# Kernel tuning notes

Measured on AMD Instinct MI355X. Metric: run time of the kernel, lower is better.

The kernel has to match this reference:

```python
import jax, jax.numpy as jnp
import numpy as np

N = 5000       # num_vertices
E = 160000     # num edges (avg degree 32)
F = 256        # per-node feature width
T = 8          # T_train iterative steps
LR_X = 0.1
N_INTERNAL = 2500


def setup_inputs() -> dict:
    key = jax.random.key(0)
    k1, k2, k3 = jax.random.split(key, 3)
    values = jax.random.normal(k1, (N, F), dtype=jnp.float32)
    w = jax.random.normal(k2, (N, N), dtype=jnp.float32) * 0.05  # nn.init.normal_(std=0.05)
    edge_index = jax.random.randint(k3, (2, E), 0, N, dtype=jnp.int64)
    internal_indices = jnp.arange(N_INTERNAL, dtype=jnp.int64)
    return {"values": values, "w": w, "edge_index": edge_index,
            "internal_indices": internal_indices}


def reference(values, w, edge_index, internal_indices):
    # PyG source_to_target flow: x_j = x[edge_index[0]], aggregate at edge_index[1]
    src, dst = edge_index[0], edge_index[1]
    w_e = w[src, dst][:, None]            # [E,1] gathered edge weights
    lr = jnp.float32(LR_X)

    def step(vals, _):
        # prediction_mp: scatter_add of w * tanh(x_j) into dst
        pred = jax.ops.segment_sum(w_e * jnp.tanh(vals[src]), dst, num_segments=N)
        err = vals - pred                 # errors[:] = values - prediction
        # gradx_mp: scatter_add of w * dfdx(err_j); dfdx(tanh) = 1 - tanh^2
        t = jnp.tanh(err[src])
        gradx = err - jax.ops.segment_sum(w_e * (1.0 - t * t), dst, num_segments=N)
        # values[internal] -= lr_x * dEdx[internal]  (train=True mask)
        vals = vals.at[internal_indices].add(-lr * gradx[internal_indices])
        return vals, None

    vals, _ = jax.lax.scan(step, values, None, length=T)
    return vals
```

## Files before the change

kernel.cpp:

```cpp
#include <hip/hip_runtime.h>
#include <hip/hip_bf16.h>

#define FDIM 256
#define F2   128
#define T_STEPS 8
#define LR_X 0.1f
#define EXT_BIT (1 << 24)

typedef __hip_bfloat162 bf2;

__device__ __forceinline__ float ftanh(float x) {
    float ax = fabsf(x);
    float z  = __expf(-2.f * ax);
    float t  = (1.f - z) * __builtin_amdgcn_rcpf(1.f + z);
    return copysignf(t, x);
}
__device__ __forceinline__ float2 bf22f(const bf2 v) {
    return make_float2(__bfloat162float(v.x), __bfloat162float(v.y));
}
__device__ __forceinline__ bf2 f22bf(float x, float y) {
    bf2 r; r.x = __float2bfloat16(x); r.y = __float2bfloat16(y); return r;
}


__global__ void k_count_init(const int* __restrict__ dst, int* __restrict__ cnt, int E,
                             const float* __restrict__ vin, float* __restrict__ vals,
                             bf2* __restrict__ th2, int NF2, int gE) {
    const int b = (int)blockIdx.x;
    if (b < gE) {
        int e = b * 256 + (int)threadIdx.x;
        if (e < E) atomicAdd(&cnt[dst[e]], 1);
    } else {
        int i = (b - gE) * 256 + (int)threadIdx.x;
        if (i < NF2) {
            float2 v = ((const float2*)vin)[i];
            ((float2*)vals)[i] = v;
            th2[i] = f22bf(ftanh(v.x), ftanh(v.y));
        }
    }
}

__global__ __launch_bounds__(1024) void k_scan(int* cntcur, int* start, int n) {
    __shared__ int sdata[1024];
    int running = 0;
    for (int base = 0; base < n + 1; base += 1024) {
        int i = base + (int)threadIdx.x;
        int v = (i < n) ? cntcur[i] : 0;
        sdata[threadIdx.x] = v;
        __syncthreads();
        for (int off = 1; off < 1024; off <<= 1) {
            int t = ((int)threadIdx.x >= off) ? sdata[threadIdx.x - off] : 0;
            __syncthreads();
            sdata[threadIdx.x] += t;
            __syncthreads();
        }
        int incl = sdata[threadIdx.x];
        int total = sdata[1023];
        if (i <= n) {
            int excl = running + incl - v;
            start[i] = excl;
            if (i < n) cntcur[i] = excl;
        }
        running += total;
        __syncthreads();
    }
}

__global__ void k_fill(const int* __restrict__ src, const int* __restrict__ dst,
                       int* __restrict__ cursor, int* __restrict__ keyT,
                       int* __restrict__ colS, int E, int NI) {
    int e = blockIdx.x * blockDim.x + threadIdx.x;
    if (e >= E) return;
    int sc = src[e];
    int p = atomicAdd(&cursor[dst[e]], 1);
    keyT[p] = ((sc >= NI) ? EXT_BIT : 0) | e;
    colS[p] = sc;
}

__global__ __launch_bounds__(256) void k_rank_scatter(
    const int* __restrict__ keyT, const int* __restrict__ colS,
    const int* __restrict__ start, const float* __restrict__ w,
    int* __restrict__ col, float* __restrict__ wv, int* __restrict__ mid,
    int nRows, int N) {
    const int wid  = (int)((blockIdx.x * blockDim.x + threadIdx.x) >> 6);
    const int lane = (int)(threadIdx.x & 63);
    if (wid >= nRows) return;
    const int s = start[wid], e = start[wid + 1];
    int nInt = 0;
    for (int i = s + lane; i < e; i += 64) {
        const int myk = keyT[i];
        int rank = 0;
        for (int j = s; j < e; ++j)
            rank += (keyT[j] < myk) ? 1 : 0;
        const int pos = s + rank;
        const int sc  = colS[i];
        col[pos] = sc * F2;
        wv[pos]  = w[(size_t)sc * N + wid];
        nInt += (myk < EXT_BIT) ? 1 : 0;
    }
    for (int off = 1; off < 64; off <<= 1)
        nInt += __shfl_xor(nInt, off);
    if (lane == 0) mid[wid] = s + nInt;
}


__device__ __forceinline__ void gather_acc(
    const int* __restrict__ col, const float* __restrict__ wv,
    const bf2* __restrict__ src2, int s, int e, int lane, int f,
    float& ax, float& ay, float& bx, float& by) {
    for (int base = s; base < e; base += 64) {
        const int n = min(64, e - base);
        int c = 0; float ww = 0.f;
        if (lane < n) { c = col[base + lane]; ww = wv[base + lane]; }
        int j = 0;
        for (; j + 2 <= n; j += 2) {
            const int   c0 = __shfl(c, j),  c1 = __shfl(c, j + 1);
            const float w0 = __shfl(ww, j), w1 = __shfl(ww, j + 1);
            const float2 t0 = bf22f(src2[c0 + f]);
            const float2 t1 = bf22f(src2[c1 + f]);
            ax = fmaf(w0, t0.x, ax); ay = fmaf(w0, t0.y, ay);
            bx = fmaf(w1, t1.x, bx); by = fmaf(w1, t1.y, by);
        }
        for (; j < n; ++j) {
            const int c0 = __shfl(c, j); const float w0 = __shfl(ww, j);
            const float2 t0 = bf22f(src2[c0 + f]);
            ax = fmaf(w0, t0.x, ax); ay = fmaf(w0, t0.y, ay);
        }
    }
}

__global__ __launch_bounds__(F2) void k_pred_first(
    const int* __restrict__ start, const int* __restrict__ mid,
    const int* __restrict__ col, const float* __restrict__ wv,
    const float2* __restrict__ vals2, float2* __restrict__ predc2,
    const bf2* __restrict__ th2, float2* __restrict__ err2,
    bf2* __restrict__ dd2, int NI) {
    const int d = (int)blockIdx.x;
    const int f = (int)threadIdx.x;
    const int lane = f & 63;
    const int s = start[d], m = mid[d], e = start[d + 1];
    float ix = 0.f, iy = 0.f, jx = 0.f, jy = 0.f;
    float xx = 0.f, xy = 0.f, yx = 0.f, yy = 0.f;
    gather_acc(col, wv, th2, s, m, lane, f, ix, iy, jx, jy);
    gather_acc(col, wv, th2, m, e, lane, f, xx, xy, yx, yy);
    const int idx = d * F2 + f;
    const float pcx = xx + yx, pcy = xy + yy;
    predc2[idx] = make_float2(pcx, pcy);
    const float2 v = vals2[idx];
    const float ex = v.x - (pcx + ix + jx);
    const float ey = v.y - (pcy + iy + jy);
    if (d < NI) err2[idx] = make_float2(ex, ey);
    const float ux = ftanh(ex), uy = ftanh(ey);
    dd2[idx] = f22bf(1.f - ux * ux, 1.f - uy * uy);
}

__global__ __launch_bounds__(F2) void k_pred(
    const int* __restrict__ start, const int* __restrict__ mid,
    const int* __restrict__ col, const float* __restrict__ wv,
    const float2* __restrict__ vals2, const float2* __restrict__ predc2,
    const bf2* __restrict__ th2, float2* __restrict__ err2,
    bf2* __restrict__ dd2, int NI) {
    const int d = (int)blockIdx.x;
    const int f = (int)threadIdx.x;
    const int lane = f & 63;
    const int s = start[d], m = mid[d];
    float ax = 0.f, ay = 0.f, bx = 0.f, by = 0.f;
    gather_acc(col, wv, th2, s, m, lane, f, ax, ay, bx, by);
    const int idx = d * F2 + f;
    const float2 pc = predc2[idx];
    const float2 v  = vals2[idx];
    const float ex = v.x - (pc.x + ax + bx);
    const float ey = v.y - (pc.y + ay + by);
    if (d < NI) err2[idx] = make_float2(ex, ey);
    const float ux = ftanh(ex), uy = ftanh(ey);
    dd2[idx] = f22bf(1.f - ux * ux, 1.f - uy * uy);
}

__global__ __launch_bounds__(F2) void k_grad(
    const int* __restrict__ start, const int* __restrict__ col,
    const float* __restrict__ wv, const float2* __restrict__ err2,
    const bf2* __restrict__ dd2, float2* __restrict__ vals2,
    bf2* __restrict__ th2) {
    const int d = (int)blockIdx.x;
    const int f = (int)threadIdx.x;
    const int lane = f & 63;
    const int s = start[d], e = start[d + 1];
    float ax = 0.f, ay = 0.f, bx = 0.f, by = 0.f;
    gather_acc(col, wv, dd2, s, e, lane, f, ax, ay, bx, by);
    const int idx = d * F2 + f;
    const float2 er = err2[idx];
    const float2 v  = vals2[idx];
    const float nx = v.x - LR_X * (er.x - (ax + bx));
    const float ny = v.y - LR_X * (er.y - (ay + by));
    vals2[idx] = make_float2(nx, ny);
    th2[idx] = f22bf(ftanh(nx), ftanh(ny));
}


extern "C" void kernel_launch(void* const* d_in, const int* in_sizes, int n_in,
                              void* d_out, int out_size, void* d_ws, size_t ws_size,
                              hipStream_t stream) {
    const float* values = (const float*)d_in[0];
    const float* w      = (const float*)d_in[1];
    const int*   edge   = (const int*)d_in[2];
    const int NF = in_sizes[0];
    const int N  = NF / FDIM;
    const int E  = in_sizes[2] / 2;
    const int NI = in_sizes[3];
    const int NF2 = NF / 2;
    const int* srcp = edge;
    const int* dstp = edge + E;
    float* vals = (float*)d_out;

    char* ws = (char*)d_ws;
    size_t off = 0;
    auto alloc = [&](size_t bytes) {
        void* p = ws + off;
        off = (off + bytes + 255) & ~(size_t)255;
        return p;
    };
    int*   start = (int*)  alloc((size_t)(N + 1) * sizeof(int));
    int*   cur   = (int*)  alloc((size_t)N * sizeof(int));
    int*   mid   = (int*)  alloc((size_t)N * sizeof(int));
    int*   keyT  = (int*)  alloc((size_t)E * sizeof(int));
    int*   colS  = (int*)  alloc((size_t)E * sizeof(int));
    int*   col   = (int*)  alloc((size_t)E * sizeof(int));
    float* wv    = (float*)alloc((size_t)E * sizeof(float));
    bf2*   th2   = (bf2*)  alloc((size_t)NF2 * sizeof(bf2));
    bf2*   dd2   = (bf2*)  alloc((size_t)NF2 * sizeof(bf2));
    float* err   = (float*)alloc((size_t)NF * sizeof(float));
    float* predc = (float*)alloc((size_t)NF * sizeof(float));
    (void)ws_size; (void)n_in; (void)out_size;

    float2* vals2  = (float2*)vals;
    float2* err2   = (float2*)err;
    float2* predc2 = (float2*)predc;

    hipMemsetAsync(cur, 0, (size_t)N * sizeof(int), stream);
    const int gE   = (E + 255) / 256;
    const int gNF2 = (NF2 + 255) / 256;
    k_count_init<<<gE + gNF2, 256, 0, stream>>>(dstp, cur, E, values, vals, th2, NF2, gE);
    k_scan<<<1, 1024, 0, stream>>>(cur, start, N);
    k_fill<<<gE, 256, 0, stream>>>(srcp, dstp, cur, keyT, colS, E, NI);
    k_rank_scatter<<<(N + 3) / 4, 256, 0, stream>>>(keyT, colS, start, w, col, wv, mid, N, N);

    for (int t = 0; t < T_STEPS; ++t) {
        if (t == 0)
            k_pred_first<<<N, F2, 0, stream>>>(start, mid, col, wv, vals2, predc2, th2, err2, dd2, NI);
        else
            k_pred<<<N, F2, 0, stream>>>(start, mid, col, wv, vals2, predc2, th2, err2, dd2, NI);
        k_grad<<<NI, F2, 0, stream>>>(start, col, wv, err2, dd2, vals2, th2);
    }
}
```

Measured before the change: 241.3 us.

## Replace CSR build with fixed-capacity per-row buckets and pack col/weight pairs

Drops the prefix-scan and separate fill kernels by scattering edges directly into fixed CAP=256 slots per destination row, using the atomic count as the slot index. Column index and edge weight are packed into one int2 so the gather loads a single 8-byte value, and the step kernels now run two rows per 256-thread block. This removes two setup launches and one serial single-block scan, at the cost of a larger, sparser workspace. It silently overflows if any row's in-degree exceeds 256.

Measured after the change: 221.5 us. 1.09x faster.

```diff
diff --git a/kernel.cpp b/kernel.cpp
--- a/kernel.cpp
+++ b/kernel.cpp
@@ -3,6 +3,7 @@
 
 #define FDIM 256
 #define F2   128
+#define CAP  256
 #define T_STEPS 8
 #define LR_X 0.1f
 #define EXT_BIT (1 << 24)
@@ -23,13 +24,21 @@
 }
 
 
-__global__ void k_count_init(const int* __restrict__ dst, int* __restrict__ cnt, int E,
-                             const float* __restrict__ vin, float* __restrict__ vals,
-                             bf2* __restrict__ th2, int NF2, int gE) {
+__global__ void k_fill_init(const int* __restrict__ src, const int* __restrict__ dst,
+                            int* __restrict__ cnt, int* __restrict__ keyT,
+                            int* __restrict__ colS, int E, int NI,
+                            const float* __restrict__ vin, float* __restrict__ vals,
+                            bf2* __restrict__ th2, int NF2, int gE) {
     const int b = (int)blockIdx.x;
     if (b < gE) {
         int e = b * 256 + (int)threadIdx.x;
-        if (e < E) atomicAdd(&cnt[dst[e]], 1);
+        if (e < E) {
+            int sc = src[e];
+            int d  = dst[e];
+            int p  = atomicAdd(&cnt[d], 1);
+            keyT[d * CAP + p] = ((sc >= NI) ? EXT_BIT : 0) | e;
+            colS[d * CAP + p] = sc;
+        }
     } else {
         int i = (b - gE) * 256 + (int)threadIdx.x;
         if (i < NF2) {
@@ -40,78 +49,42 @@
     }
 }
 
-__global__ __launch_bounds__(1024) void k_scan(int* cntcur, int* start, int n) {
-    __shared__ int sdata[1024];
-    int running = 0;
-    for (int base = 0; base < n + 1; base += 1024) {
-        int i = base + (int)threadIdx.x;
-        int v = (i < n) ? cntcur[i] : 0;
-        sdata[threadIdx.x] = v;
-        __syncthreads();
-        for (int off = 1; off < 1024; off <<= 1) {
-            int t = ((int)threadIdx.x >= off) ? sdata[threadIdx.x - off] : 0;
-            __syncthreads();
-            sdata[threadIdx.x] += t;
-            __syncthreads();
-        }
-        int incl = sdata[threadIdx.x];
-        int total = sdata[1023];
-        if (i <= n) {
-            int excl = running + incl - v;
-            start[i] = excl;
-            if (i < n) cntcur[i] = excl;
-        }
-        running += total;
-        __syncthreads();
-    }
-}
-
-__global__ void k_fill(const int* __restrict__ src, const int* __restrict__ dst,
-                       int* __restrict__ cursor, int* __restrict__ keyT,
-                       int* __restrict__ colS, int E, int NI) {
-    int e = blockIdx.x * blockDim.x + threadIdx.x;
-    if (e >= E) return;
-    int sc = src[e];
-    int p = atomicAdd(&cursor[dst[e]], 1);
-    keyT[p] = ((sc >= NI) ? EXT_BIT : 0) | e;
-    colS[p] = sc;
-}
-
 __global__ __launch_bounds__(256) void k_rank_scatter(
     const int* __restrict__ keyT, const int* __restrict__ colS,
-    const int* __restrict__ start, const float* __restrict__ w,
-    int* __restrict__ col, float* __restrict__ wv, int* __restrict__ mid,
-    int nRows, int N) {
+    const int* __restrict__ cnt, const float* __restrict__ w,
+    int2* __restrict__ cw, int* __restrict__ nint, int nRows, int N) {
     const int wid  = (int)((blockIdx.x * blockDim.x + threadIdx.x) >> 6);
     const int lane = (int)(threadIdx.x & 63);
     if (wid >= nRows) return;
-    const int s = start[wid], e = start[wid + 1];
+    const int base = wid * CAP;
+    const int deg  = cnt[wid];
     int nInt = 0;
-    for (int i = s + lane; i < e; i += 64) {
-        const int myk = keyT[i];
+    for (int i = lane; i < deg; i += 64) {
+        const int myk = keyT[base + i];
         int rank = 0;
-        for (int j = s; j < e; ++j)
-            rank += (keyT[j] < myk) ? 1 : 0;
-        const int pos = s + rank;
-        const int sc  = colS[i];
-        col[pos] = sc * F2;
-        wv[pos]  = w[(size_t)sc * N + wid];
+        for (int j = 0; j < deg; ++j)
+            rank += (keyT[base + j] < myk) ? 1 : 0;
+        const int sc = colS[base + i];
+        int2 p;
+        p.x = sc * F2;
+        p.y = __float_as_int(w[(size_t)sc * N + wid]);
+        cw[base + rank] = p;
         nInt += (myk < EXT_BIT) ? 1 : 0;
     }
     for (int off = 1; off < 64; off <<= 1)
         nInt += __shfl_xor(nInt, off);
-    if (lane == 0) mid[wid] = s + nInt;
+    if (lane == 0) nint[wid] = nInt;
 }
 
 
 __device__ __forceinline__ void gather_acc(
-    const int* __restrict__ col, const float* __restrict__ wv,
-    const bf2* __restrict__ src2, int s, int e, int lane, int f,
+    const int2* __restrict__ cw, const bf2* __restrict__ src2,
+    int s, int e, int lane, int f,
     float& ax, float& ay, float& bx, float& by) {
     for (int base = s; base < e; base += 64) {
         const int n = min(64, e - base);
         int c = 0; float ww = 0.f;
-        if (lane < n) { c = col[base + lane]; ww = wv[base + lane]; }
+        if (lane < n) { int2 p = cw[base + lane]; c = p.x; ww = __int_as_float(p.y); }
         int j = 0;
         for (; j + 2 <= n; j += 2) {
             const int   c0 = __shfl(c, j),  c1 = __shfl(c, j + 1);
@@ -129,65 +102,68 @@
     }
 }
 
-__global__ __launch_bounds__(F2) void k_pred_first(
-    const int* __restrict__ start, const int* __restrict__ mid,
-    const int* __restrict__ col, const float* __restrict__ wv,
-    const float2* __restrict__ vals2, float2* __restrict__ predc2,
-    const bf2* __restrict__ th2, float2* __restrict__ err2,
-    bf2* __restrict__ dd2, int NI) {
-    const int d = (int)blockIdx.x;
-    const int f = (int)threadIdx.x;
-    const int lane = f & 63;
-    const int s = start[d], m = mid[d], e = start[d + 1];
+__global__ __launch_bounds__(256) void k_pred_first(
+    const int* __restrict__ nint, const int* __restrict__ cnt,
+    const int2* __restrict__ cw, const float2* __restrict__ vals2,
+    float2* __restrict__ predc2, const bf2* __restrict__ th2,
+    float2* __restrict__ err2, bf2* __restrict__ dd2, int N, int NI) {
+    const int r = (int)blockIdx.x * 2 + ((int)threadIdx.x >> 7);
+    if (r >= N) return;
+    const int f = (int)threadIdx.x & 127;
+    const int lane = (int)threadIdx.x & 63;
+    const int base = r * CAP;
+    const int m = base + nint[r], e = base + cnt[r];
     float ix = 0.f, iy = 0.f, jx = 0.f, jy = 0.f;
     float xx = 0.f, xy = 0.f, yx = 0.f, yy = 0.f;
-    gather_acc(col, wv, th2, s, m, lane, f, ix, iy, jx, jy);
-    gather_acc(col, wv, th2, m, e, lane, f, xx, xy, yx, yy);
-    const int idx = d * F2 + f;
+    gather_acc(cw, th2, base, m, lane, f, ix, iy, jx, jy);
+    gather_acc(cw, th2, m, e, lane, f, xx, xy, yx, yy);
+    const int idx = r * F2 + f;
     const float pcx = xx + yx, pcy = xy + yy;
     predc2[idx] = make_float2(pcx, pcy);
     const float2 v = vals2[idx];
     const float ex = v.x - (pcx + ix + jx);
     const float ey = v.y - (pcy + iy + jy);
-    if (d < NI) err2[idx] = make_float2(ex, ey);
+    if (r < NI) err2[idx] = make_float2(ex, ey);
     const float ux = ftanh(ex), uy = ftanh(ey);
     dd2[idx] = f22bf(1.f - ux * ux, 1.f - uy * uy);
 }
 
-__global__ __launch_bounds__(F2) void k_pred(
-    const int* __restrict__ start, const int* __restrict__ mid,
-    const int* __restrict__ col, const float* __restrict__ wv,
+__global__ __launch_bounds__(256) void k_pred(
+    const int* __restrict__ nint, const int2* __restrict__ cw,
     const float2* __restrict__ vals2, const float2* __restrict__ predc2,
     const bf2* __restrict__ th2, float2* __restrict__ err2,
-    bf2* __restrict__ dd2, int NI) {
-    const int d = (int)blockIdx.x;
-    const int f = (int)threadIdx.x;
-    const int lane = f & 63;
-    const int s = start[d], m = mid[d];
+    bf2* __restrict__ dd2, int N, int NI) {
+    const int r = (int)blockIdx.x * 2 + ((int)threadIdx.x >> 7);
+    if (r >= N) return;
+    const int f = (int)threadIdx.x & 127;
+    const int lane = (int)threadIdx.x & 63;
+    const int base = r * CAP;
+    const int m = base + nint[r];
     float ax = 0.f, ay = 0.f, bx = 0.f, by = 0.f;
-    gather_acc(col, wv, th2, s, m, lane, f, ax, ay, bx, by);
-    const int idx = d * F2 + f;
+    gather_acc(cw, th2, base, m, lane, f, ax, ay, bx, by);
+    const int idx = r * F2 + f;
     const float2 pc = predc2[idx];
     const float2 v  = vals2[idx];
     const float ex = v.x - (pc.x + ax + bx);
     const float ey = v.y - (pc.y + ay + by);
-    if (d < NI) err2[idx] = make_float2(ex, ey);
+    if (r < NI) err2[idx] = make_float2(ex, ey);
     const float ux = ftanh(ex), uy = ftanh(ey);
     dd2[idx] = f22bf(1.f - ux * ux, 1.f - uy * uy);
 }
 
-__global__ __launch_bounds__(F2) void k_grad(
-    const int* __restrict__ start, const int* __restrict__ col,
-    const float* __restrict__ wv, const float2* __restrict__ err2,
-    const bf2* __restrict__ dd2, float2* __restrict__ vals2,
-    bf2* __restrict__ th2) {
-    const int d = (int)blockIdx.x;
-    const int f = (int)threadIdx.x;
-    const int lane = f & 63;
-    const int s = start[d], e = start[d + 1];
+__global__ __launch_bounds__(256) void k_grad(
+    const int* __restrict__ cnt, const int2* __restrict__ cw,
+    const float2* __restrict__ err2, const bf2* __restrict__ dd2,
+    float2* __restrict__ vals2, bf2* __restrict__ th2, int NI) {
+    const int r = (int)blockIdx.x * 2 + ((int)threadIdx.x >> 7);
+    if (r >= NI) return;
+    const int f = (int)threadIdx.x & 127;
+    const int lane = (int)threadIdx.x & 63;
+    const int base = r * CAP;
+    const int e = base + cnt[r];
     float ax = 0.f, ay = 0.f, bx = 0.f, by = 0.f;
-    gather_acc(col, wv, dd2, s, e, lane, f, ax, ay, bx, by);
-    const int idx = d * F2 + f;
+    gather_acc(cw, dd2, base, e, lane, f, ax, ay, bx, by);
+    const int idx = r * F2 + f;
     const float2 er = err2[idx];
     const float2 v  = vals2[idx];
     const float nx = v.x - LR_X * (er.x - (ax + bx));
@@ -219,15 +195,13 @@
         off = (off + bytes + 255) & ~(size_t)255;
         return p;
     };
-    int*   start = (int*)  alloc((size_t)(N + 1) * sizeof(int));
-    int*   cur   = (int*)  alloc((size_t)N * sizeof(int));
-    int*   mid   = (int*)  alloc((size_t)N * sizeof(int));
-    int*   keyT  = (int*)  alloc((size_t)E * sizeof(int));
-    int*   colS  = (int*)  alloc((size_t)E * sizeof(int));
-    int*   col   = (int*)  alloc((size_t)E * sizeof(int));
-    float* wv    = (float*)alloc((size_t)E * sizeof(float));
-    bf2*   th2   = (bf2*)  alloc((size_t)NF2 * sizeof(bf2));
-    bf2*   dd2   = (bf2*)  alloc((size_t)NF2 * sizeof(bf2));
+    int*  cnt  = (int*) alloc((size_t)N * sizeof(int));
+    int*  nint = (int*) alloc((size_t)N * sizeof(int));
+    int*  keyT = (int*) alloc((size_t)N * CAP * sizeof(int));
+    int*  colS = (int*) alloc((size_t)N * CAP * sizeof(int));
+    int2* cw   = (int2*)alloc((size_t)N * CAP * sizeof(int2));
+    bf2*  th2  = (bf2*) alloc((size_t)NF2 * sizeof(bf2));
+    bf2*  dd2  = (bf2*) alloc((size_t)NF2 * sizeof(bf2));
     float* err   = (float*)alloc((size_t)NF * sizeof(float));
     float* predc = (float*)alloc((size_t)NF * sizeof(float));
     (void)ws_size; (void)n_in; (void)out_size;
@@ -236,19 +210,20 @@
     float2* err2   = (float2*)err;
     float2* predc2 = (float2*)predc;
 
-    hipMemsetAsync(cur, 0, (size_t)N * sizeof(int), stream);
+    hipMemsetAsync(cnt, 0, (size_t)N * sizeof(int), stream);
     const int gE   = (E + 255) / 256;
     const int gNF2 = (NF2 + 255) / 256;
-    k_count_init<<<gE + gNF2, 256, 0, stream>>>(dstp, cur, E, values, vals, th2, NF2, gE);
-    k_scan<<<1, 1024, 0, stream>>>(cur, start, N);
-    k_fill<<<gE, 256, 0, stream>>>(srcp, dstp, cur, keyT, colS, E, NI);
-    k_rank_scatter<<<(N + 3) / 4, 256, 0, stream>>>(keyT, colS, start, w, col, wv, mid, N, N);
-
+    k_fill_init<<<gE + gNF2, 256, 0, stream>>>(srcp, dstp, cnt, keyT, colS, E, NI,
+                                               values, vals, th2, NF2, gE);
+    k_rank_scatter<<<(N + 3) / 4, 256, 0, stream>>>(keyT, colS, cnt, w, cw, nint, N, N);
+
+    const int gP = (N + 1) / 2;
+    const int gG = (NI + 1) / 2;
     for (int t = 0; t < T_STEPS; ++t) {
         if (t == 0)
-            k_pred_first<<<N, F2, 0, stream>>>(start, mid, col, wv, vals2, predc2, th2, err2, dd2, NI);
+            k_pred_first<<<gP, 256, 0, stream>>>(nint, cnt, cw, vals2, predc2, th2, err2, dd2, N, NI);
         else
-            k_pred<<<N, F2, 0, stream>>>(start, mid, col, wv, vals2, predc2, th2, err2, dd2, NI);
-        k_grad<<<NI, F2, 0, stream>>>(start, col, wv, err2, dd2, vals2, th2);
-    }
-}
+            k_pred<<<gP, 256, 0, stream>>>(nint, cw, vals2, predc2, th2, err2, dd2, N, NI);
+        k_grad<<<gG, 256, 0, stream>>>(cnt, cw, err2, dd2, vals2, th2, NI);
+    }
+}
```
